# Kernel tuning notes

Measured on AMD Instinct MI355X. Metric: run time of the kernel, lower is better.

Reference implementation:

```python
import jax, jax.numpy as jnp
import numpy as np

N = 100000      # nodes
E = 1600000     # edges
IN_DIM = 256
H = 128         # hidden_mlp == hidden_gnn
Z = 32          # latent_dim
HD = 128        # hidden_dec


def _lin(k, fan_in, fan_out):
    # torch nn.Linear default init: U(-1/sqrt(fan_in), 1/sqrt(fan_in))
    kw, kb = jax.random.split(k)
    lim = 1.0 / np.sqrt(fan_in)
    W = jax.random.uniform(kw, (fan_in, fan_out), jnp.float32, -lim, lim)
    b = jax.random.uniform(kb, (fan_out,), jnp.float32, -lim, lim)
    return W, b


def setup_inputs() -> dict:
    key = jax.random.key(0)
    ks = jax.random.split(key, 16)
    x = jax.random.normal(ks[0], (N, IN_DIM), jnp.float32)
    edge_index = jax.random.randint(ks[1], (2, E), 0, N, jnp.int64)
    edge_attr = jax.random.uniform(ks[2], (E,), jnp.float32)

    W1, b1 = _lin(ks[3], IN_DIM, H)       # encoder mlp layer 1
    W2, b2 = _lin(ks[4], H, H)            # encoder mlp layer 2
    Wrel1, brel1 = _lin(ks[5], H, H)      # gnn1 lin_rel
    Wroot1, _ = _lin(ks[6], H, H)         # gnn1 lin_root (no bias)
    Wrel2, brel2 = _lin(ks[7], H, H)      # gnn2 lin_rel
    Wroot2, _ = _lin(ks[8], H, H)         # gnn2 lin_root
    Wmu, bmu = _lin(ks[9], H, Z)
    Wlv, blv = _lin(ks[10], H, Z)
    Wd1, bd1 = _lin(ks[11], Z, HD)
    Wd2, bd2 = _lin(ks[12], HD, IN_DIM)
    eps = jax.random.normal(ks[13], (N, Z), jnp.float32)  # reparam noise (fixed)

    return dict(x=x, edge_index=edge_index, edge_attr=edge_attr,
                W1=W1, b1=b1, W2=W2, b2=b2,
                Wrel1=Wrel1, brel1=brel1, Wroot1=Wroot1,
                Wrel2=Wrel2, brel2=brel2, Wroot2=Wroot2,
                Wmu=Wmu, bmu=bmu, Wlv=Wlv, blv=blv,
                Wd1=Wd1, bd1=bd1, Wd2=Wd2, bd2=bd2, eps=eps)


def _graph_conv(h, src, dst, w, Wrel, brel, Wroot):
    # PyG GraphConv (aggr='add'): out_i = lin_rel(sum_{j->i} w_ji * h_j) + lin_root(h_i)
    msgs = h[src] * w[:, None]                       # [E, H] gather
    agg = jax.ops.segment_sum(msgs, dst, num_segments=N)  # [N, H] scatter-add
    return agg @ Wrel + brel + h @ Wroot


def reference(x, edge_index, edge_attr,
              W1, b1, W2, b2,
              Wrel1, brel1, Wroot1,
              Wrel2, brel2, Wroot2,
              Wmu, bmu, Wlv, blv,
              Wd1, bd1, Wd2, bd2, eps):
    src, dst = edge_index[0], edge_index[1]
    # encoder MLP
    h = jax.nn.relu(x @ W1 + b1)
    h = jax.nn.relu(h @ W2 + b2)
    # two GraphConv message-passing layers with ReLU
    h = jax.nn.relu(_graph_conv(h, src, dst, edge_attr, Wrel1, brel1, Wroot1))
    h = jax.nn.relu(_graph_conv(h, src, dst, edge_attr, Wrel2, brel2, Wroot2))
    # heads
    mu = h @ Wmu + bmu
    logvar = h @ Wlv + blv
    # reparameterize with fixed eps
    z = mu + eps * jnp.exp(0.5 * logvar)
    # decoder MLP
    x_recon = jax.nn.relu(z @ Wd1 + bd1) @ Wd2 + bd2
    return x_recon, mu, logvar, z
```

## Files before the change

kernel.cpp:

```cpp
#include <hip/hip_runtime.h>
#include <math.h>

#define NN 100000
#define EE 1600000
#define NB 1563

typedef _Float16 f16;
typedef __attribute__((ext_vector_type(2))) _Float16 f16x2;
typedef __attribute__((ext_vector_type(8))) _Float16 f16x8;
typedef __attribute__((ext_vector_type(4))) float f32x4;
typedef unsigned int u32;

__device__ __forceinline__ float frelu(float v){ return v > 0.f ? v : 0.f; }

__device__ __forceinline__ f32x4 mfma16(f16x8 a, f16x8 b, f32x4 c){
    return __builtin_amdgcn_mfma_f32_16x16x32_f16(a, b, c, 0, 0, 0);
}

__device__ __forceinline__ int2 nt_load_int2(const int2* p){
    long long v = __builtin_nontemporal_load((const long long*)p);
    int2 r; r.x = (int)(v & 0xFFFFFFFFll); r.y = (int)(v >> 32);
    return r;
}

__global__ __launch_bounds__(256) void hist_pack(const int* __restrict__ dst,
                                                 int* __restrict__ blockhist,
                                                 const float* __restrict__ W1,
                                                 const float* __restrict__ W2,
                                                 const float* __restrict__ Wrel1,
                                                 const float* __restrict__ Wroot1,
                                                 const float* __restrict__ Wrel2,
                                                 const float* __restrict__ Wroot2,
                                                 const float* __restrict__ Wd1,
                                                 const float* __restrict__ Wd2,
                                                 const float* __restrict__ Wmu,
                                                 const float* __restrict__ Wlv,
                                                 f16* __restrict__ pack)
{
    __shared__ int cntS[NB];
    const int t = threadIdx.x;
    if (blockIdx.x < 250) {
        const int blk = blockIdx.x;
        for (int i = t; i < NB; i += 256) cntS[i] = 0;
        __syncthreads();
        const int ebase = blk * 6400;
        #pragma unroll
        for (int i = 0; i < 25; i++) {
            int k = dst[ebase + i * 256 + t] >> 6;
            atomicAdd(&cntS[k], 1);
        }
        __syncthreads();
        for (int i = t; i < NB; i += 256)
            blockhist[blk * NB + i] = cntS[i];
        return;
    }
    int tt = (blockIdx.x - 250) * 256 + t;
    float v;
    if (tt < 32768) {
        int l = tt;
        int j = l & 7, lane = (l >> 3) & 63, ct = (l >> 9) & 7, kk = l >> 12;
        int k = kk * 32 + ((lane >> 4) << 3) + j, c = (ct << 4) + (lane & 15);
        v = W1[k * 128 + c];
    } else if (tt < 49152) {
        int l = tt - 32768;
        int j = l & 7, lane = (l >> 3) & 63, ct = (l >> 9) & 7, kk = l >> 12;
        int k = kk * 32 + ((lane >> 4) << 3) + j, c = (ct << 4) + (lane & 15);
        v = W2[k * 128 + c];
    } else if (tt < 81920) {
        int l = tt - 49152;
        int j = l & 7, lane = (l >> 3) & 63, ct = (l >> 9) & 7, kk = l >> 12;
        int k = kk * 32 + ((lane >> 4) << 3) + j, c = (ct << 4) + (lane & 15);
        v = (k < 128) ? Wrel1[k * 128 + c] : Wroot1[(k - 128) * 128 + c];
    } else if (tt < 114688) {
        int l = tt - 81920;
        int j = l & 7, lane = (l >> 3) & 63, ct = (l >> 9) & 7, kk = l >> 12;
        int k = kk * 32 + ((lane >> 4) << 3) + j, c = (ct << 4) + (lane & 15);
        v = (k < 128) ? Wrel2[k * 128 + c] : Wroot2[(k - 128) * 128 + c];
    } else if (tt < 118784) {
        int l = tt - 114688;
        int j = l & 7, lane = (l >> 3) & 63, ct = (l >> 9) & 7;
        int k = ((lane >> 4) << 3) + j, c = (ct << 4) + (lane & 15);
        v = Wd1[k * 128 + c];
    } else if (tt < 151552) {
        int l = tt - 118784;
        int j = l & 7, lane = (l >> 3) & 63, ct = (l >> 9) & 15, kk = l >> 13;
        int k = kk * 32 + ((lane >> 4) << 3) + j, c = (ct << 4) + (lane & 15);
        v = Wd2[k * 256 + c];
    } else {
        int l = tt - 151552;
        int j = l & 7, lane = (l >> 3) & 63, ct = (l >> 9) & 3, kk = l >> 11;
        int k = kk * 32 + ((lane >> 4) << 3) + j, c = (ct << 4) + (lane & 15);
        v = (c < 32) ? Wmu[k * 32 + c] : Wlv[k * 32 + (c - 32)];
    }
    pack[tt] = (f16)v;
}

__global__ __launch_bounds__(256) void colscan(int* __restrict__ blockhist,
                                               int* __restrict__ totals)
{
    __shared__ int lds[256];
    const int t = threadIdx.x, k = blockIdx.x;
    int v = (t < 250) ? blockhist[t * NB + k] : 0;
    lds[t] = v;
    __syncthreads();
    for (int off = 1; off < 256; off <<= 1) {
        int y = (t >= off) ? lds[t - off] : 0;
        __syncthreads();
        lds[t] += y;
        __syncthreads();
    }
    if (t < 250) blockhist[t * NB + k] = lds[t] - v;
    if (t == 255) totals[k] = lds[255];
}

__global__ __launch_bounds__(256) void scatter(const int* __restrict__ src,
                                               const int* __restrict__ dst,
                                               const float* __restrict__ ea,
                                               const int* __restrict__ totals,
                                               const int* __restrict__ blockhist,
                                               int* __restrict__ bs_g,
                                               int2* __restrict__ tmp)
{
    __shared__ int bsS[NB + 1];
    __shared__ int tmpS[256];
    __shared__ int carryS;
    __shared__ int prefS[NB];
    __shared__ int cntS[NB];
    const int t = threadIdx.x, blk = blockIdx.x;
    if (t == 0) carryS = 0;
    __syncthreads();
    for (int c = 0; c < 7; c++) {
        int idx = c * 256 + t;
        int val = (idx < NB) ? totals[idx] : 0;
        tmpS[t] = val;
        __syncthreads();
        for (int off = 1; off < 256; off <<= 1) {
            int y = (t >= off) ? tmpS[t - off] : 0;
            __syncthreads();
            tmpS[t] += y;
            __syncthreads();
        }
        if (idx < NB) bsS[idx] = carryS + tmpS[t] - val;
        __syncthreads();
        if (t == 255) carryS += tmpS[255];
        __syncthreads();
    }
    if (t == 0) bsS[NB] = carryS;
    for (int i = t; i < NB; i += 256) {
        prefS[i] = blockhist[blk * NB + i];
        cntS[i] = 0;
    }
    __syncthreads();
    if (blk == 0)
        for (int i = t; i < NB + 1; i += 256) bs_g[i] = bsS[i];
    const int ebase = blk * 6400;
    #pragma unroll
    for (int i = 0; i < 25; i++) {
        int e = ebase + i * 256 + t;
        int d = dst[e];
        int k = d >> 6;
        int rank = atomicAdd(&cntS[k], 1);
        int pos = bsS[k] + prefS[k] + rank;
        tmp[pos] = make_int2(src[e] | ((d & 63) << 17), __float_as_int(ea[e]));
    }
}

__global__ __launch_bounds__(256) void bucket_sort(const int2* __restrict__ tmp,
                                                   const int* __restrict__ bs_g,
                                                   int2* __restrict__ pairs,
                                                   int* __restrict__ offsets,
                                                   int* __restrict__ counts)
{
    __shared__ int hist[64], excl[64], cursor[64];
    const int t = threadIdx.x, k = blockIdx.x;
    const int start = bs_g[k], end = bs_g[k + 1];
    if (t < 64) hist[t] = 0;
    __syncthreads();
    for (int i = start + t; i < end; i += 256)
        atomicAdd(&hist[(tmp[i].x >> 17) & 63], 1);
    __syncthreads();
    if (t == 0) {
        int run = 0;
        #pragma unroll
        for (int j = 0; j < 64; j++) { excl[j] = run; cursor[j] = run; run += hist[j]; }
    }
    __syncthreads();
    for (int i = start + t; i < end; i += 256) {
        int2 e = tmp[i];
        int local = (e.x >> 17) & 63;
        int rank = atomicAdd(&cursor[local], 1);
        pairs[start + rank] = make_int2(e.x & 0x1FFFF, e.y);
    }
    if (t < 64) {
        int node = (k << 6) + t;
        if (node < NN) {
            counts[node]  = hist[t];
            offsets[node] = start + excl[t] + hist[t];
        }
    }
}

__global__ __launch_bounds__(256) void agg_q(const f16* __restrict__ h,
                                             const int2* __restrict__ pairs,
                                             const int* __restrict__ offsets,
                                             const int* __restrict__ counts,
                                             f16* __restrict__ out)
{
    const int gt   = blockIdx.x * 256 + threadIdx.x;
    const int node = gt >> 4;
    const int ch   = gt & 15;
    const int end  = offsets[node];
    int i = end - counts[node];
    float acc[8];
    #pragma unroll
    for (int j = 0; j < 8; j++) acc[j] = 0.f;
    const uint4* __restrict__ h16 = (const uint4*)h;
    for (; i + 2 <= end; i += 2) {
        int2 p0 = nt_load_int2(pairs + i);
        int2 p1 = nt_load_int2(pairs + i + 1);
        uint4 r0 = h16[(size_t)p0.x * 16 + ch];
        uint4 r1 = h16[(size_t)p1.x * 16 + ch];
        float w0 = __int_as_float(p0.y), w1 = __int_as_float(p1.y);
        const f16* e0 = (const f16*)&r0;
        const f16* e1 = (const f16*)&r1;
        #pragma unroll
        for (int j = 0; j < 8; j++) acc[j] = fmaf(w0, (float)e0[j], acc[j]);
        #pragma unroll
        for (int j = 0; j < 8; j++) acc[j] = fmaf(w1, (float)e1[j], acc[j]);
    }
    if (i < end) {
        int2 p0 = nt_load_int2(pairs + i);
        uint4 r0 = h16[(size_t)p0.x * 16 + ch];
        float w0 = __int_as_float(p0.y);
        const f16* e0 = (const f16*)&r0;
        #pragma unroll
        for (int j = 0; j < 8; j++) acc[j] = fmaf(w0, (float)e0[j], acc[j]);
    }
    union { f16 hh[8]; uint4 u; } cv;
    #pragma unroll
    for (int j = 0; j < 8; j++) cv.hh[j] = (f16)acc[j];
    ((uint4*)out)[(size_t)node * 16 + ch] = cv.u;
}

template<int C>
__device__ __forceinline__ void stage_tile(const float* __restrict__ src, int nbase,
                                           f16* lds, int ldr, int colofs)
{
    const int t = threadIdx.x;
    #pragma unroll
    for (int i = 0; i < (64 * C / 4) / 256; i++) {
        int elem = t + i * 256;
        int row = elem / (C / 4);
        int c4  = elem % (C / 4);
        int srow = nbase + row; if (srow >= NN) srow = NN - 1;
        float4 v = *(const float4*)(src + (size_t)srow * C + c4 * 4);
        union { f16 h[4]; uint2 u; } cv;
        cv.h[0] = (f16)v.x; cv.h[1] = (f16)v.y; cv.h[2] = (f16)v.z; cv.h[3] = (f16)v.w;
        *(uint2*)&lds[row * ldr + colofs + c4 * 4] = cv.u;
    }
}

template<int C>
__device__ __forceinline__ void stage_tile_f16(const f16* __restrict__ src, int nbase,
                                               f16* lds, int ldr, int colofs)
{
    const int t = threadIdx.x;
    #pragma unroll
    for (int i = 0; i < (64 * C / 4) / 256; i++) {
        int elem = t + i * 256;
        int row = elem / (C / 4);
        int c4  = elem % (C / 4);
        int srow = nbase + row; if (srow >= NN) srow = NN - 1;
        uint2 v = *(const uint2*)(src + (size_t)srow * C + c4 * 4);
        *(uint2*)&lds[row * ldr + colofs + c4 * 4] = v;
    }
}

template<int K, int CT>
__device__ __forceinline__ void wave_gemm(const f16* lds, int ldr,
                                          const f16x8* __restrict__ wp, f32x4 acc[CT])
{
    const int lane = threadIdx.x & 63;
    const int wrow = (threadIdx.x >> 6) * 16;
    const int arow = wrow + (lane & 15);
    const int kofs = (lane >> 4) << 3;
    #pragma unroll
    for (int kk = 0; kk < K / 32; kk++) {
        f16x8 a = *(const f16x8*)&lds[arow * ldr + kk * 32 + kofs];
        #pragma unroll
        for (int ct = 0; ct < CT; ct++) {
            f16x8 b = wp[(kk * CT + ct) * 64 + lane];
            acc[ct] = mfma16(a, b, acc[ct]);
        }
    }
}

template<int CT>
__device__ __forceinline__ void zacc(f32x4 acc[CT])
{
    #pragma unroll
    for (int ct = 0; ct < CT; ct++) acc[ct] = f32x4{0.f, 0.f, 0.f, 0.f};
}

template<int CT, bool RELU>
__device__ __forceinline__ void store_f32(float* __restrict__ dst, int OUTC, int nbase,
                                          const float* __restrict__ bias, f32x4 acc[CT])
{
    const int lane = threadIdx.x & 63;
    const int wrow = (threadIdx.x >> 6) * 16;
    #pragma unroll
    for (int ct = 0; ct < CT; ct++) {
        int c = ct * 16 + (lane & 15);
        float bv = bias[c];
        #pragma unroll
        for (int r = 0; r < 4; r++) {
            int node = nbase + wrow + ((lane >> 4) << 2) + r;
            if (node < NN) {
                float v = acc[ct][r] + bv;
                if (RELU) v = frelu(v);
                dst[(size_t)node * OUTC + c] = v;
            }
        }
    }
}

template<int CT, bool RELU>
__device__ __forceinline__ void store_f16g(f16* __restrict__ dst, int OUTC, int nbase,
                                           const float* __restrict__ bias, f32x4 acc[CT])
{
    const int lane = threadIdx.x & 63;
    const int wrow = (threadIdx.x >> 6) * 16;
    #pragma unroll
    for (int ct = 0; ct < CT; ct++) {
        int c = ct * 16 + (lane & 15);
        float bv = bias[c];
        #pragma unroll
        for (int r = 0; r < 4; r++) {
            int node = nbase + wrow + ((lane >> 4) << 2) + r;
            if (node < NN) {
                float v = acc[ct][r] + bv;
                if (RELU) v = frelu(v);
                dst[(size_t)node * OUTC + c] = (f16)v;
            }
        }
    }
}

template<int CT>
__device__ __forceinline__ void store_lds_f16(f16* lds, int ldr,
                                              const float* __restrict__ bias, f32x4 acc[CT])
{
    const int lane = threadIdx.x & 63;
    const int wrow = (threadIdx.x >> 6) * 16;
    #pragma unroll
    for (int ct = 0; ct < CT; ct++) {
        int c = ct * 16 + (lane & 15);
        float bv = bias[c];
        #pragma unroll
        for (int r = 0; r < 4; r++) {
            int row = wrow + ((lane >> 4) << 2) + r;
            lds[row * ldr + c] = (f16)frelu(acc[ct][r] + bv);
        }
    }
}

__global__ __launch_bounds__(256) void enc_mfma(const float* __restrict__ x,
                                                const f16x8* __restrict__ wp1,
                                                const f16x8* __restrict__ wp2,
                                                const float* __restrict__ b1,
                                                const float* __restrict__ b2,
                                                f16* __restrict__ out)
{
    __shared__ __align__(16) f16 xs[64 * 264];
    __shared__ __align__(16) f16 h1[64 * 136];
    const int nbase = blockIdx.x * 64;
    stage_tile<256>(x, nbase, xs, 264, 0);
    __syncthreads();
    f32x4 acc[8];
    zacc<8>(acc);
    wave_gemm<256, 8>(xs, 264, wp1, acc);
    store_lds_f16<8>(h1, 136, b1, acc);
    __syncthreads();
    zacc<8>(acc);
    wave_gemm<128, 8>(h1, 136, wp2, acc);
    store_f16g<8, true>(out, 128, nbase, b2, acc);
}

__global__ __launch_bounds__(256) void conv_mfma(const f16* __restrict__ agg,
                                                 const f16* __restrict__ h,
                                                 const f16x8* __restrict__ wp,
                                                 const float* __restrict__ brel,
                                                 f16* __restrict__ out)
{
    __shared__ __align__(16) f16 as_[64 * 264];
    const int nbase = blockIdx.x * 64;
    stage_tile_f16<128>(agg, nbase, as_, 264, 0);
    stage_tile_f16<128>(h,   nbase, as_, 264, 128);
    __syncthreads();
    f32x4 acc[8];
    zacc<8>(acc);
    wave_gemm<256, 8>(as_, 264, wp, acc);
    store_f16g<8, true>(out, 128, nbase, brel, acc);
}

__global__ __launch_bounds__(256) void heads_mfma(const f16* __restrict__ h,
                                                  const f16x8* __restrict__ wp,
                                                  const float* __restrict__ bmu,
                                                  const float* __restrict__ blv,
                                                  const float* __restrict__ eps,
                                                  float* __restrict__ out)
{
    __shared__ __align__(16) f16 hs[64 * 136];
    __shared__ __align__(16) float muS[64 * 32];
    __shared__ __align__(16) float lvS[64 * 32];
    const int nbase = blockIdx.x * 64;
    stage_tile_f16<128>(h, nbase, hs, 136, 0);
    __syncthreads();
    f32x4 acc[4];
    zacc<4>(acc);
    wave_gemm<128, 4>(hs, 136, wp, acc);
    const int lane = threadIdx.x & 63;
    const int wrow = (threadIdx.x >> 6) * 16;
    #pragma unroll
    for (int ct = 0; ct < 4; ct++) {
        int c = ct * 16 + (lane & 15);
        bool ismu = (c < 32);
        int cc = c & 31;
        float bv = ismu ? bmu[cc] : blv[cc];
        float* gbase = out + (ismu ? (size_t)25600000 : (size_t)28800000);
        float* sb = ismu ? muS : lvS;
        #pragma unroll
        for (int r = 0; r < 4; r++) {
            int row = wrow + ((lane >> 4) << 2) + r;
            int node = nbase + row;
            float v = acc[ct][r] + bv;
            sb[row * 32 + cc] = v;
            if (node < NN) gbase[(size_t)node * 32 + cc] = v;
        }
    }
    __syncthreads();
    {
        const int node = threadIdx.x >> 2;
        const int ch0  = (threadIdx.x & 3) * 8;
        const int gn = nbase + node;
        if (gn < NN) {
            const size_t g = (size_t)gn * 32 + ch0;
            float4 e0 = *(const float4*)(eps + g);
            float4 e1 = *(const float4*)(eps + g + 4);
            const float* mu = &muS[node * 32 + ch0];
            const float* lv = &lvS[node * 32 + ch0];
            float4 z0, z1;
            z0.x = fmaf(e0.x, expf(0.5f * lv[0]), mu[0]);
            z0.y = fmaf(e0.y, expf(0.5f * lv[1]), mu[1]);
            z0.z = fmaf(e0.z, expf(0.5f * lv[2]), mu[2]);
            z0.w = fmaf(e0.w, expf(0.5f * lv[3]), mu[3]);
            z1.x = fmaf(e1.x, expf(0.5f * lv[4]), mu[4]);
            z1.y = fmaf(e1.y, expf(0.5f * lv[5]), mu[5]);
            z1.z = fmaf(e1.z, expf(0.5f * lv[6]), mu[6]);
            z1.w = fmaf(e1.w, expf(0.5f * lv[7]), mu[7]);
            *(float4*)(out + 32000000 + g) = z0;
            *(float4*)(out + 32000000 + g + 4) = z1;
        }
    }
}

__global__ __launch_bounds__(256) void dec_mfma(const float* __restrict__ z,
                                                const f16x8* __restrict__ wp1,
                                                const float* __restrict__ bd1,
                                                const f16x8* __restrict__ wp2,
                                                const float* __restrict__ bd2,
                                                float* __restrict__ out)
{
    __shared__ __align__(16) f16 zs[64 * 40];
    __shared__ __align__(16) f16 hd[64 * 136];
    const int nbase = blockIdx.x * 64;
    stage_tile<32>(z, nbase, zs, 40, 0);
    __syncthreads();
    f32x4 acc[8];
    zacc<8>(acc);
    wave_gemm<32, 8>(zs, 40, wp1, acc);
    store_lds_f16<8>(hd, 136, bd1, acc);
    __syncthreads();
    f32x4 acc2[16];
    zacc<16>(acc2);
    wave_gemm<128, 16>(hd, 136, wp2, acc2);
    store_f32<16, false>(out, 256, nbase, bd2, acc2);
}

extern "C" void kernel_launch(void* const* d_in, const int* in_sizes, int n_in,
                              void* d_out, int out_size, void* d_ws, size_t ws_size,
                              hipStream_t stream)
{
    const float* x     = (const float*)d_in[0];
    const int*   ei    = (const int*)d_in[1];
    const float* ea    = (const float*)d_in[2];
    const float* W1    = (const float*)d_in[3];
    const float* b1    = (const float*)d_in[4];
    const float* W2    = (const float*)d_in[5];
    const float* b2    = (const float*)d_in[6];
    const float* Wrel1 = (const float*)d_in[7];
    const float* brel1 = (const float*)d_in[8];
    const float* Wroot1= (const float*)d_in[9];
    const float* Wrel2 = (const float*)d_in[10];
    const float* brel2 = (const float*)d_in[11];
    const float* Wroot2= (const float*)d_in[12];
    const float* Wmu   = (const float*)d_in[13];
    const float* bmu   = (const float*)d_in[14];
    const float* Wlv   = (const float*)d_in[15];
    const float* blv   = (const float*)d_in[16];
    const float* Wd1   = (const float*)d_in[17];
    const float* bd1   = (const float*)d_in[18];
    const float* Wd2   = (const float*)d_in[19];
    const float* bd2   = (const float*)d_in[20];
    const float* eps   = (const float*)d_in[21];
    float* out = (float*)d_out;

    char* ws = (char*)d_ws;
    int*  totals    = (int*) (ws);
    int*  blockhist = (int*) (ws + 8192);
    int*  bs_g      = (int*) (ws + 1571200);
    int2* tmp       = (int2*)(ws + 1577472);
    int2* pairs     = (int2*)(ws + 14377472);
    int*  offsets   = (int*) (ws + 27177472);
    int*  counts    = (int*) (ws + 27577472);
    f16*  pack      = (f16*) (ws + 27977472);
    f16*  B0        = (f16*) (ws + 28311552);
    f16*  B1        = (f16*) (ws + 53911552);

    const f16x8* wp_enc1  = (const f16x8*)(pack);
    const f16x8* wp_enc2  = (const f16x8*)(pack + 32768);
    const f16x8* wp_conv1 = (const f16x8*)(pack + 49152);
    const f16x8* wp_conv2 = (const f16x8*)(pack + 81920);
    const f16x8* wp_dec1  = (const f16x8*)(pack + 114688);
    const f16x8* wp_dec2  = (const f16x8*)(pack + 118784);
    const f16x8* wp_heads = (const f16x8*)(pack + 151552);

    const int* src = ei;
    const int* dst = ei + EE;

    hist_pack<<<874, 256, 0, stream>>>(dst, blockhist, W1, W2, Wrel1, Wroot1,
                                       Wrel2, Wroot2, Wd1, Wd2, Wmu, Wlv, pack);
    colscan<<<NB, 256, 0, stream>>>(blockhist, totals);
    scatter<<<250, 256, 0, stream>>>(src, dst, ea, totals, blockhist, bs_g, tmp);
    bucket_sort<<<NB, 256, 0, stream>>>(tmp, bs_g, pairs, offsets, counts);

    enc_mfma<<<1563, 256, 0, stream>>>(x, wp_enc1, wp_enc2, b1, b2, B0);
    agg_q<<<6250, 256, 0, stream>>>(B0, pairs, offsets, counts, B1);
    conv_mfma<<<1563, 256, 0, stream>>>(B1, B0, wp_conv1, brel1, B1);
    agg_q<<<6250, 256, 0, stream>>>(B1, pairs, offsets, counts, B0);
    conv_mfma<<<1563, 256, 0, stream>>>(B0, B1, wp_conv2, brel2, B0);
    heads_mfma<<<1563, 256, 0, stream>>>(B0, wp_heads, bmu, blv, eps, out);
    dec_mfma<<<1563, 256, 0, stream>>>(out + 32000000, wp_dec1, bd1, wp_dec2, bd2, out);
}
```

Before: 427.3 us.

## Merge column scan with encoder MLP kernel and unroll aggregation by four

The column-scan blocks and the encoder MLP blocks now run in one launch, with block index choosing the role. The encoder does not depend on the sort, so it can overlap with the latency-bound scan and one kernel launch is removed. The edge-aggregation loop is also unrolled from two edges to four to keep more gathers in flight. The combined kernel reserves the encoder's larger LDS for the scan blocks too, which may lower their occupancy, and the wider unroll adds register pressure.

Measured after the change: 402.9 us. -5.7%, faster.

```diff
diff --git a/kernel.cpp b/kernel.cpp
--- a/kernel.cpp
+++ b/kernel.cpp
@@ -95,22 +95,168 @@
     pack[tt] = (f16)v;
 }
 
-__global__ __launch_bounds__(256) void colscan(int* __restrict__ blockhist,
-                                               int* __restrict__ totals)
-{
-    __shared__ int lds[256];
-    const int t = threadIdx.x, k = blockIdx.x;
-    int v = (t < 250) ? blockhist[t * NB + k] : 0;
-    lds[t] = v;
-    __syncthreads();
-    for (int off = 1; off < 256; off <<= 1) {
-        int y = (t >= off) ? lds[t - off] : 0;
+template<int C>
+__device__ __forceinline__ void stage_tile(const float* __restrict__ src, int nbase,
+                                           f16* lds, int ldr, int colofs)
+{
+    const int t = threadIdx.x;
+    #pragma unroll
+    for (int i = 0; i < (64 * C / 4) / 256; i++) {
+        int elem = t + i * 256;
+        int row = elem / (C / 4);
+        int c4  = elem % (C / 4);
+        int srow = nbase + row; if (srow >= NN) srow = NN - 1;
+        float4 v = *(const float4*)(src + (size_t)srow * C + c4 * 4);
+        union { f16 h[4]; uint2 u; } cv;
+        cv.h[0] = (f16)v.x; cv.h[1] = (f16)v.y; cv.h[2] = (f16)v.z; cv.h[3] = (f16)v.w;
+        *(uint2*)&lds[row * ldr + colofs + c4 * 4] = cv.u;
+    }
+}
+
+template<int C>
+__device__ __forceinline__ void stage_tile_f16(const f16* __restrict__ src, int nbase,
+                                               f16* lds, int ldr, int colofs)
+{
+    const int t = threadIdx.x;
+    #pragma unroll
+    for (int i = 0; i < (64 * C / 4) / 256; i++) {
+        int elem = t + i * 256;
+        int row = elem / (C / 4);
+        int c4  = elem % (C / 4);
+        int srow = nbase + row; if (srow >= NN) srow = NN - 1;
+        uint2 v = *(const uint2*)(src + (size_t)srow * C + c4 * 4);
+        *(uint2*)&lds[row * ldr + colofs + c4 * 4] = v;
+    }
+}
+
+template<int K, int CT>
+__device__ __forceinline__ void wave_gemm(const f16* lds, int ldr,
+                                          const f16x8* __restrict__ wp, f32x4 acc[CT])
+{
+    const int lane = threadIdx.x & 63;
+    const int wrow = (threadIdx.x >> 6) * 16;
+    const int arow = wrow + (lane & 15);
+    const int kofs = (lane >> 4) << 3;
+    #pragma unroll
+    for (int kk = 0; kk < K / 32; kk++) {
+        f16x8 a = *(const f16x8*)&lds[arow * ldr + kk * 32 + kofs];
+        #pragma unroll
+        for (int ct = 0; ct < CT; ct++) {
+            f16x8 b = wp[(kk * CT + ct) * 64 + lane];
+            acc[ct] = mfma16(a, b, acc[ct]);
+        }
+    }
+}
+
+template<int CT>
+__device__ __forceinline__ void zacc(f32x4 acc[CT])
+{
+    #pragma unroll
+    for (int ct = 0; ct < CT; ct++) acc[ct] = f32x4{0.f, 0.f, 0.f, 0.f};
+}
+
+template<int CT, bool RELU>
+__device__ __forceinline__ void store_f32(float* __restrict__ dst, int OUTC, int nbase,
+                                          const float* __restrict__ bias, f32x4 acc[CT])
+{
+    const int lane = threadIdx.x & 63;
+    const int wrow = (threadIdx.x >> 6) * 16;
+    #pragma unroll
+    for (int ct = 0; ct < CT; ct++) {
+        int c = ct * 16 + (lane & 15);
+        float bv = bias[c];
+        #pragma unroll
+        for (int r = 0; r < 4; r++) {
+            int node = nbase + wrow + ((lane >> 4) << 2) + r;
+            if (node < NN) {
+                float v = acc[ct][r] + bv;
+                if (RELU) v = frelu(v);
+                dst[(size_t)node * OUTC + c] = v;
+            }
+        }
+    }
+}
+
+template<int CT, bool RELU>
+__device__ __forceinline__ void store_f16g(f16* __restrict__ dst, int OUTC, int nbase,
+                                           const float* __restrict__ bias, f32x4 acc[CT])
+{
+    const int lane = threadIdx.x & 63;
+    const int wrow = (threadIdx.x >> 6) * 16;
+    #pragma unroll
+    for (int ct = 0; ct < CT; ct++) {
+        int c = ct * 16 + (lane & 15);
+        float bv = bias[c];
+        #pragma unroll
+        for (int r = 0; r < 4; r++) {
+            int node = nbase + wrow + ((lane >> 4) << 2) + r;
+            if (node < NN) {
+                float v = acc[ct][r] + bv;
+                if (RELU) v = frelu(v);
+                dst[(size_t)node * OUTC + c] = (f16)v;
+            }
+        }
+    }
+}
+
+template<int CT>
+__device__ __forceinline__ void store_lds_f16(f16* lds, int ldr,
+                                              const float* __restrict__ bias, f32x4 acc[CT])
+{
+    const int lane = threadIdx.x & 63;
+    const int wrow = (threadIdx.x >> 6) * 16;
+    #pragma unroll
+    for (int ct = 0; ct < CT; ct++) {
+        int c = ct * 16 + (lane & 15);
+        float bv = bias[c];
+        #pragma unroll
+        for (int r = 0; r < 4; r++) {
+            int row = wrow + ((lane >> 4) << 2) + r;
+            lds[row * ldr + c] = (f16)frelu(acc[ct][r] + bv);
+        }
+    }
+}
+
+__global__ __launch_bounds__(256) void colscan_enc(int* __restrict__ blockhist,
+                                                   int* __restrict__ totals,
+                                                   const float* __restrict__ x,
+                                                   const f16x8* __restrict__ wp1,
+                                                   const f16x8* __restrict__ wp2,
+                                                   const float* __restrict__ b1,
+                                                   const float* __restrict__ b2,
+                                                   f16* __restrict__ out)
+{
+    __shared__ __align__(16) f16 shbuf[64 * 264 + 64 * 136];
+    const int t = threadIdx.x;
+    if (blockIdx.x < NB) {
+        int* lds = (int*)shbuf;
+        const int k = blockIdx.x;
+        int v = (t < 250) ? blockhist[t * NB + k] : 0;
+        lds[t] = v;
         __syncthreads();
-        lds[t] += y;
-        __syncthreads();
-    }
-    if (t < 250) blockhist[t * NB + k] = lds[t] - v;
-    if (t == 255) totals[k] = lds[255];
+        for (int off = 1; off < 256; off <<= 1) {
+            int y = (t >= off) ? lds[t - off] : 0;
+            __syncthreads();
+            lds[t] += y;
+            __syncthreads();
+        }
+        if (t < 250) blockhist[t * NB + k] = lds[t] - v;
+        if (t == 255) totals[k] = lds[255];
+        return;
+    }
+    f16* xs = shbuf;
+    f16* h1 = shbuf + 64 * 264;
+    const int nbase = (blockIdx.x - NB) * 64;
+    stage_tile<256>(x, nbase, xs, 264, 0);
+    __syncthreads();
+    f32x4 acc[8];
+    zacc<8>(acc);
+    wave_gemm<256, 8>(xs, 264, wp1, acc);
+    store_lds_f16<8>(h1, 136, b1, acc);
+    __syncthreads();
+    zacc<8>(acc);
+    wave_gemm<128, 8>(h1, 136, wp2, acc);
+    store_f16g<8, true>(out, 128, nbase, b2, acc);
 }
 
 __global__ __launch_bounds__(256) void scatter(const int* __restrict__ src,
@@ -215,20 +361,31 @@
     #pragma unroll
     for (int j = 0; j < 8; j++) acc[j] = 0.f;
     const uint4* __restrict__ h16 = (const uint4*)h;
-    for (; i + 2 <= end; i += 2) {
+    for (; i + 4 <= end; i += 4) {
         int2 p0 = nt_load_int2(pairs + i);
         int2 p1 = nt_load_int2(pairs + i + 1);
+        int2 p2 = nt_load_int2(pairs + i + 2);
+        int2 p3 = nt_load_int2(pairs + i + 3);
         uint4 r0 = h16[(size_t)p0.x * 16 + ch];
         uint4 r1 = h16[(size_t)p1.x * 16 + ch];
+        uint4 r2 = h16[(size_t)p2.x * 16 + ch];
+        uint4 r3 = h16[(size_t)p3.x * 16 + ch];
         float w0 = __int_as_float(p0.y), w1 = __int_as_float(p1.y);
+        float w2 = __int_as_float(p2.y), w3 = __int_as_float(p3.y);
         const f16* e0 = (const f16*)&r0;
         const f16* e1 = (const f16*)&r1;
+        const f16* e2 = (const f16*)&r2;
+        const f16* e3 = (const f16*)&r3;
         #pragma unroll
         for (int j = 0; j < 8; j++) acc[j] = fmaf(w0, (float)e0[j], acc[j]);
         #pragma unroll
         for (int j = 0; j < 8; j++) acc[j] = fmaf(w1, (float)e1[j], acc[j]);
-    }
-    if (i < end) {
+        #pragma unroll
+        for (int j = 0; j < 8; j++) acc[j] = fmaf(w2, (float)e2[j], acc[j]);
+        #pragma unroll
+        for (int j = 0; j < 8; j++) acc[j] = fmaf(w3, (float)e3[j], acc[j]);
+    }
+    for (; i < end; ++i) {
         int2 p0 = nt_load_int2(pairs + i);
         uint4 r0 = h16[(size_t)p0.x * 16 + ch];
         float w0 = __int_as_float(p0.y);
@@ -240,150 +397,6 @@
     #pragma unroll
     for (int j = 0; j < 8; j++) cv.hh[j] = (f16)acc[j];
     ((uint4*)out)[(size_t)node * 16 + ch] = cv.u;
-}
-
-template<int C>
-__device__ __forceinline__ void stage_tile(const float* __restrict__ src, int nbase,
-                                           f16* lds, int ldr, int colofs)
-{
-    const int t = threadIdx.x;
-    #pragma unroll
-    for (int i = 0; i < (64 * C / 4) / 256; i++) {
-        int elem = t + i * 256;
-        int row = elem / (C / 4);
-        int c4  = elem % (C / 4);
-        int srow = nbase + row; if (srow >= NN) srow = NN - 1;
-        float4 v = *(const float4*)(src + (size_t)srow * C + c4 * 4);
-        union { f16 h[4]; uint2 u; } cv;
-        cv.h[0] = (f16)v.x; cv.h[1] = (f16)v.y; cv.h[2] = (f16)v.z; cv.h[3] = (f16)v.w;
-        *(uint2*)&lds[row * ldr + colofs + c4 * 4] = cv.u;
-    }
-}
-
-template<int C>
-__device__ __forceinline__ void stage_tile_f16(const f16* __restrict__ src, int nbase,
-                                               f16* lds, int ldr, int colofs)
-{
-    const int t = threadIdx.x;
-    #pragma unroll
-    for (int i = 0; i < (64 * C / 4) / 256; i++) {
-        int elem = t + i * 256;
-        int row = elem / (C / 4);
-        int c4  = elem % (C / 4);
-        int srow = nbase + row; if (srow >= NN) srow = NN - 1;
-        uint2 v = *(const uint2*)(src + (size_t)srow * C + c4 * 4);
-        *(uint2*)&lds[row * ldr + colofs + c4 * 4] = v;
-    }
-}
-
-template<int K, int CT>
-__device__ __forceinline__ void wave_gemm(const f16* lds, int ldr,
-                                          const f16x8* __restrict__ wp, f32x4 acc[CT])
-{
-    const int lane = threadIdx.x & 63;
-    const int wrow = (threadIdx.x >> 6) * 16;
-    const int arow = wrow + (lane & 15);
-    const int kofs = (lane >> 4) << 3;
-    #pragma unroll
-    for (int kk = 0; kk < K / 32; kk++) {
-        f16x8 a = *(const f16x8*)&lds[arow * ldr + kk * 32 + kofs];
-        #pragma unroll
-        for (int ct = 0; ct < CT; ct++) {
-            f16x8 b = wp[(kk * CT + ct) * 64 + lane];
-            acc[ct] = mfma16(a, b, acc[ct]);
-        }
-    }
-}
-
-template<int CT>
-__device__ __forceinline__ void zacc(f32x4 acc[CT])
-{
-    #pragma unroll
-    for (int ct = 0; ct < CT; ct++) acc[ct] = f32x4{0.f, 0.f, 0.f, 0.f};
-}
-
-template<int CT, bool RELU>
-__device__ __forceinline__ void store_f32(float* __restrict__ dst, int OUTC, int nbase,
-                                          const float* __restrict__ bias, f32x4 acc[CT])
-{
-    const int lane = threadIdx.x & 63;
-    const int wrow = (threadIdx.x >> 6) * 16;
-    #pragma unroll
-    for (int ct = 0; ct < CT; ct++) {
-        int c = ct * 16 + (lane & 15);
-        float bv = bias[c];
-        #pragma unroll
-        for (int r = 0; r < 4; r++) {
-            int node = nbase + wrow + ((lane >> 4) << 2) + r;
-            if (node < NN) {
-                float v = acc[ct][r] + bv;
-                if (RELU) v = frelu(v);
-                dst[(size_t)node * OUTC + c] = v;
-            }
-        }
-    }
-}
-
-template<int CT, bool RELU>
-__device__ __forceinline__ void store_f16g(f16* __restrict__ dst, int OUTC, int nbase,
-                                           const float* __restrict__ bias, f32x4 acc[CT])
-{
-    const int lane = threadIdx.x & 63;
-    const int wrow = (threadIdx.x >> 6) * 16;
-    #pragma unroll
-    for (int ct = 0; ct < CT; ct++) {
-        int c = ct * 16 + (lane & 15);
-        float bv = bias[c];
-        #pragma unroll
-        for (int r = 0; r < 4; r++) {
-            int node = nbase + wrow + ((lane >> 4) << 2) + r;
-            if (node < NN) {
-                float v = acc[ct][r] + bv;
-                if (RELU) v = frelu(v);
-                dst[(size_t)node * OUTC + c] = (f16)v;
-            }
-        }
-    }
-}
-
-template<int CT>
-__device__ __forceinline__ void store_lds_f16(f16* lds, int ldr,
-                                              const float* __restrict__ bias, f32x4 acc[CT])
-{
-    const int lane = threadIdx.x & 63;
-    const int wrow = (threadIdx.x >> 6) * 16;
-    #pragma unroll
-    for (int ct = 0; ct < CT; ct++) {
-        int c = ct * 16 + (lane & 15);
-        float bv = bias[c];
-        #pragma unroll
-        for (int r = 0; r < 4; r++) {
-            int row = wrow + ((lane >> 4) << 2) + r;
-            lds[row * ldr + c] = (f16)frelu(acc[ct][r] + bv);
-        }
-    }
-}
-
-__global__ __launch_bounds__(256) void enc_mfma(const float* __restrict__ x,
-                                                const f16x8* __restrict__ wp1,
-                                                const f16x8* __restrict__ wp2,
-                                                const float* __restrict__ b1,
-                                                const float* __restrict__ b2,
-                                                f16* __restrict__ out)
-{
-    __shared__ __align__(16) f16 xs[64 * 264];
-    __shared__ __align__(16) f16 h1[64 * 136];
-    const int nbase = blockIdx.x * 64;
-    stage_tile<256>(x, nbase, xs, 264, 0);
-    __syncthreads();
-    f32x4 acc[8];
-    zacc<8>(acc);
-    wave_gemm<256, 8>(xs, 264, wp1, acc);
-    store_lds_f16<8>(h1, 136, b1, acc);
-    __syncthreads();
-    zacc<8>(acc);
-    wave_gemm<128, 8>(h1, 136, wp2, acc);
-    store_f16g<8, true>(out, 128, nbase, b2, acc);
 }
 
 __global__ __launch_bounds__(256) void conv_mfma(const f16* __restrict__ agg,
@@ -540,11 +553,11 @@
 
     hist_pack<<<874, 256, 0, stream>>>(dst, blockhist, W1, W2, Wrel1, Wroot1,
                                        Wrel2, Wroot2, Wd1, Wd2, Wmu, Wlv, pack);
-    colscan<<<NB, 256, 0, stream>>>(blockhist, totals);
+    colscan_enc<<<NB + 1563, 256, 0, stream>>>(blockhist, totals, x,
+                                               wp_enc1, wp_enc2, b1, b2, B0);
     scatter<<<250, 256, 0, stream>>>(src, dst, ea, totals, blockhist, bs_g, tmp);
     bucket_sort<<<NB, 256, 0, stream>>>(tmp, bs_g, pairs, offsets, counts);
 
-    enc_mfma<<<1563, 256, 0, stream>>>(x, wp_enc1, wp_enc2, b1, b2, B0);
     agg_q<<<6250, 256, 0, stream>>>(B0, pairs, offsets, counts, B1);
     conv_mfma<<<1563, 256, 0, stream>>>(B1, B0, wp_conv1, brel1, B1);
     agg_q<<<6250, 256, 0, stream>>>(B1, pairs, offsets, counts, B0);
```
